# Kernel tuning notes

Hardware: AMD Instinct MI355X
Metric: run time of the kernel (lower is better)

The kernel has to match this reference:

```python
import jax, jax.numpy as jnp
import numpy as np

B, T, C = 16, 4096, 256


def setup_inputs() -> dict:
    key = jax.random.key(0)
    kx, kl = jax.random.split(key)
    x = jax.random.normal(kx, (B, T, C), dtype=jnp.float32)
    lengths = jax.random.randint(kl, (B,), T // 2, T + 1)  # valid lengths per sample
    pool_ranges = lengths  # region to pool over; k <= pool_range guaranteed by layer/total_layers choice
    return {
        "x": x,
        "lengths": lengths,
        "pool_ranges": pool_ranges,
        "top_k": 4,
        "layer": 1,
        "total_layers": 4,
    }


def _pool_one(xb, k, pool_range):
    # xb: [T, C]; keep, per column independently, the k largest values among the
    # first pool_range rows, preserving original row order (torch kmax_pooling).
    Trows, Ccols = xb.shape
    valid = jnp.arange(Trows) < pool_range            # [T]
    vals = jnp.where(valid[:, None], xb, -jnp.inf)    # mask invalid rows to rank last
    order = jnp.argsort(-vals, axis=0)                # descending order per column
    rank = jnp.argsort(order, axis=0)                 # inverse permutation = rank of each row
    keep = (rank < k) & valid[:, None]                # [T, C] which entries survive
    pos = jnp.cumsum(keep.astype(jnp.int32), axis=0) - 1  # compacted output row per column
    idx = jnp.where(keep, pos, Trows)                 # dropped entries -> dummy row Trows
    cols = jnp.arange(Ccols)[None, :]
    out = jnp.zeros((Trows + 1, Ccols), xb.dtype).at[idx, cols].set(
        jnp.where(keep, xb, jnp.zeros((), xb.dtype))
    )
    return out[:-1]                                   # [T, C]; rows >= k are zero padding


def reference(x, lengths, pool_ranges, top_k, layer, total_layers):
    # pool_target = max(top_k, ceil((total_layers - layer)/total_layers * length))
    num = total_layers - layer
    k = jnp.maximum(top_k, (num * lengths + total_layers - 1) // total_layers)
    k = jnp.minimum(k, pool_ranges)  # topk requires k <= available rows
    results = jax.vmap(_pool_one)(x, k, pool_ranges)  # [B, T, C], zero-padded past k_i
    pool_result_ranges = k
    return results, pool_result_ranges
```

## Files before the change

kernel.cpp:

```cpp
#include <hip/hip_runtime.h>
#include <stdint.h>


constexpr int T_ROWS = 4096;
constexpr int C_COLS = 256;
constexpr int NBATCH = 16;
constexpr int NSUB   = 8;
constexpr size_t NTOT = (size_t)NBATCH * T_ROWS * C_COLS;

__device__ __forceinline__ int compute_k(const int* lengths, const int* pool_ranges,
                                         const int* p_top_k, const int* p_layer,
                                         const int* p_total, int b, int* pr_out)
{
    int pr = pool_ranges[b];
    pr = pr < 0 ? 0 : (pr > T_ROWS ? T_ROWS : pr);
    const int len   = lengths[b];
    const int top_k = p_top_k[0];
    const int tot   = p_total[0];
    const int num   = tot - p_layer[0];
    int k = (num * len + tot - 1) / tot;
    if (k < top_k) k = top_k;
    if (k > pr)    k = pr;
    *pr_out = pr;
    return k;
}

__global__ __launch_bounds__(256)
void transpose_key_kernel(const float* __restrict__ x, uint32_t* __restrict__ xT)
{
    __shared__ uint32_t tile[64][65];
    const int bid = blockIdx.x;
    const int b   = bid >> 8;
    const int tt  = (bid >> 2) & 63;
    const int ct  = bid & 3;
    const int t0  = tt * 64, c0 = ct * 64;
    const int tid = threadIdx.x;
    const int qq  = tid & 15;
    const int rr  = tid >> 4;

    #pragma unroll
    for (int it = 0; it < 4; ++it) {
        const int r = it * 16 + rr;
        const float4 v = *reinterpret_cast<const float4*>(
            x + ((size_t)(b * T_ROWS + t0 + r) << 8) + c0 + qq * 4);
        const uint32_t w4[4] = {__float_as_uint(v.x), __float_as_uint(v.y),
                                __float_as_uint(v.z), __float_as_uint(v.w)};
        #pragma unroll
        for (int j = 0; j < 4; ++j)
            tile[qq * 4 + j][r] = w4[j] ^ ((w4[j] >> 31) ? 0xFFFFFFFFu : 0x80000000u);
    }
    __syncthreads();
    #pragma unroll
    for (int it = 0; it < 4; ++it) {
        const int cl = it * 16 + rr;
        uint4 o;
        o.x = tile[cl][qq * 4 + 0];
        o.y = tile[cl][qq * 4 + 1];
        o.z = tile[cl][qq * 4 + 2];
        o.w = tile[cl][qq * 4 + 3];
        *reinterpret_cast<uint4*>(
            xT + ((size_t)(b * C_COLS + c0 + cl) << 12) + t0 + qq * 4) = o;
    }
}

__global__ __launch_bounds__(256, 4)
void kmax_select_kernel(const uint32_t* __restrict__ xT,
                        const int* __restrict__ lengths,
                        const int* __restrict__ pool_ranges,
                        const int* __restrict__ p_top_k,
                        const int* __restrict__ p_layer,
                        const int* __restrict__ p_total,
                        float* __restrict__ out,
                        float* __restrict__ ws)
{
    __shared__ uint32_t hist[4][NSUB][256];

    const int t    = threadIdx.x;
    const int lane = t & 63;
    const int wid  = t >> 6;
    const int bid  = blockIdx.x;
    const int b    = bid >> 6;
    const int cg   = bid & 63;
    const int c    = cg * 4 + wid;

    int pr;
    const int k = compute_k(lengths, pool_ranges, p_top_k, p_layer, p_total, b, &pr);

    const uint4* cp = reinterpret_cast<const uint4*>(
                          xT + ((size_t)(b * C_COLS + c) << 12)) + lane;
    const int rb = lane * 4;
    uint32_t u[64];
    uint4 pf[4];
    #pragma unroll
    for (int i = 0; i < 4; ++i) pf[i] = cp[i * 64];
    #pragma unroll
    for (int i = 0; i < 16; ++i) {
        const uint4 v = pf[i & 3];
        if (i + 4 < 16) pf[i & 3] = cp[(i + 4) * 64];
        const int rowb = i * 256 + rb;
        u[i * 4 + 0] = (rowb + 0 < pr) ? v.x : 0u;
        u[i * 4 + 1] = (rowb + 1 < pr) ? v.y : 0u;
        u[i * 4 + 2] = (rowb + 2 < pr) ? v.z : 0u;
        u[i * 4 + 3] = (rowb + 3 < pr) ? v.w : 0u;
        asm("" : "+v"(u[i*4+0]), "+v"(u[i*4+1]), "+v"(u[i*4+2]), "+v"(u[i*4+3]));
    }

    if (k > 0) {
        uint32_t* hp = &hist[wid][0][0];
        uint32_t prefix = 0u, pmask = 0u, rem = (uint32_t)k;
        const uint32_t sub = lane & (NSUB - 1);

        #pragma unroll 1
        for (int pass = 0; pass < 4; ++pass) {
            const int shift = 24 - 8 * pass;
            uint4* hp4 = reinterpret_cast<uint4*>(hp);
            const uint4 z4 = make_uint4(0u, 0u, 0u, 0u);
            #pragma unroll
            for (int z = 0; z < 8; ++z) hp4[z * 64 + lane] = z4;
            #pragma unroll
            for (int m = 0; m < 64; ++m) {
                const uint32_t ui = u[m];
                if ((ui & pmask) == prefix)
                    atomicAdd(&hp[sub * 256 + (255u - ((ui >> shift) & 255u))], 1u);
            }
            uint32_t c4[4] = {0u, 0u, 0u, 0u};
            #pragma unroll
            for (int s = 0; s < NSUB; ++s) {
                const uint4 a = *reinterpret_cast<const uint4*>(&hp[s * 256 + 4 * lane]);
                c4[0] += a.x; c4[1] += a.y; c4[2] += a.z; c4[3] += a.w;
            }
            uint32_t loc[4], ssum = 0;
            #pragma unroll
            for (int q = 0; q < 4; ++q) { loc[q] = ssum; ssum += c4[q]; }
            uint32_t incl = ssum;
            #pragma unroll
            for (int off = 1; off < 64; off <<= 1) {
                const uint32_t nb = __shfl_up(incl, (unsigned)off, 64);
                if (lane >= off) incl += nb;
            }
            const uint32_t gexcl = incl - ssum;
            uint32_t sel = 0, nrem = 0;
            bool found = false;
            #pragma unroll
            for (int q = 0; q < 4; ++q) {
                const uint32_t sbb = gexcl + loc[q];
                if (sbb < rem && sbb + c4[q] >= rem) {
                    sel   = 255u - (uint32_t)(4 * lane + q);
                    nrem  = rem - sbb;
                    found = true;
                }
            }
            const unsigned long long fm = __ballot(found);
            const int src = __ffsll(fm) - 1;
            sel  = __shfl(sel,  src, 64);
            nrem = __shfl(nrem, src, 64);
            prefix |= sel << shift;
            pmask  |= 0xFFu << shift;
            rem = nrem;
        }

        const uint32_t th = prefix, tn = rem;
        uint32_t G = 0, E = 0;
        float* dst = ws + ((size_t)(b * C_COLS + c) << 12);
        #pragma unroll
        for (int i = 0; i < 16; ++i) {
            const int rowb = i * 256 + rb;
            uint32_t gt[4], eq[4], pk = 0;
            #pragma unroll
            for (int j = 0; j < 4; ++j) {
                const uint32_t ui = u[i * 4 + j];
                gt[j] = (ui > th) ? 1u : 0u;
                eq[j] = ((rowb + j < pr) && ui == th) ? 1u : 0u;
                pk += (gt[j] << 16) | eq[j];
            }
            uint32_t incl = pk;
            #pragma unroll
            for (int off = 1; off < 64; off <<= 1) {
                const uint32_t nb = __shfl_up(incl, (unsigned)off, 64);
                if (lane >= off) incl += nb;
            }
            const uint32_t tot  = __shfl(incl, 63, 64);
            const uint32_t base = incl - pk;
            uint32_t g = G + (base >> 16), e = E + (base & 0xFFFFu);
            #pragma unroll
            for (int j = 0; j < 4; ++j) {
                if (gt[j] || (eq[j] && e < tn)) {
                    const uint32_t pos  = g + (e < tn ? e : tn);
                    const uint32_t ui   = u[i * 4 + j];
                    const uint32_t bits = ui ^ ((ui >> 31) ? 0x80000000u : 0xFFFFFFFFu);
                    dst[pos] = __uint_as_float(bits);
                }
                g += gt[j];
                e += eq[j];
            }
            G += tot >> 16;
            E += tot & 0xFFFFu;
        }
    }

    if (cg == 0 && t == 0)
        out[NTOT + (size_t)b] = (float)k;
}

__global__ __launch_bounds__(256)
void finalize_kernel(const float* __restrict__ ws,
                     const int* __restrict__ lengths,
                     const int* __restrict__ pool_ranges,
                     const int* __restrict__ p_top_k,
                     const int* __restrict__ p_layer,
                     const int* __restrict__ p_total,
                     float* __restrict__ out)
{
    __shared__ float tile[64][65];
    const int bid  = blockIdx.x;
    const int b    = bid >> 8;
    const int pt   = (bid >> 2) & 63;
    const int ct   = bid & 3;
    const int pos0 = pt * 64, c0 = ct * 64;

    int pr;
    const int k = compute_k(lengths, pool_ranges, p_top_k, p_layer, p_total, b, &pr);

    const int tid = threadIdx.x;
    const int qq  = tid & 15;
    const int rr  = tid >> 4;
    float4* out4 = reinterpret_cast<float4*>(out);
    const float4 z4 = make_float4(0.f, 0.f, 0.f, 0.f);

    if (pos0 < k) {
        const float4* ws4 = reinterpret_cast<const float4*>(ws);
        #pragma unroll
        for (int it = 0; it < 4; ++it) {
            const int cl = it * 16 + rr;
            const float4 v = ws4[((size_t)(b * C_COLS + c0 + cl) << 10)
                                 + (pos0 >> 2) + qq];
            tile[cl][qq * 4 + 0] = v.x;
            tile[cl][qq * 4 + 1] = v.y;
            tile[cl][qq * 4 + 2] = v.z;
            tile[cl][qq * 4 + 3] = v.w;
        }
        __syncthreads();
        #pragma unroll
        for (int it = 0; it < 4; ++it) {
            const int r = it * 16 + rr;
            float4 v;
            v.x = tile[qq * 4 + 0][r];
            v.y = tile[qq * 4 + 1][r];
            v.z = tile[qq * 4 + 2][r];
            v.w = tile[qq * 4 + 3][r];
            if (pos0 + r >= k) v = z4;
            out4[((size_t)(b * T_ROWS + pos0 + r) << 6) + (c0 >> 2) + qq] = v;
        }
    } else {
        #pragma unroll
        for (int it = 0; it < 4; ++it) {
            const int r = it * 16 + rr;
            out4[((size_t)(b * T_ROWS + pos0 + r) << 6) + (c0 >> 2) + qq] = z4;
        }
    }
}

extern "C" void kernel_launch(void* const* d_in, const int* in_sizes, int n_in,
                              void* d_out, int out_size, void* d_ws, size_t ws_size,
                              hipStream_t stream)
{
    const float* x            = (const float*)d_in[0];
    const int*   lengths      = (const int*)d_in[1];
    const int*   pool_ranges  = (const int*)d_in[2];
    const int*   top_k        = (const int*)d_in[3];
    const int*   layer        = (const int*)d_in[4];
    const int*   total_layers = (const int*)d_in[5];
    float*       out          = (float*)d_out;
    float*       ws           = (float*)d_ws;

    hipLaunchKernelGGL(transpose_key_kernel, dim3(4096), dim3(256), 0, stream,
                       x, (uint32_t*)ws);
    hipLaunchKernelGGL(kmax_select_kernel, dim3(1024), dim3(256), 0, stream,
                       (const uint32_t*)ws, lengths, pool_ranges,
                       top_k, layer, total_layers, out, ws);
    hipLaunchKernelGGL(finalize_kernel, dim3(4096), dim3(256), 0, stream,
                       ws, lengths, pool_ranges, top_k, layer, total_layers, out);
}
```

Baseline: 90.70 us.

## Split each column's radix select across two wavefronts with shared histograms

Each column is now processed by two wavefronts (512-thread blocks), each holding half the rows in registers (32 values instead of 64). The two halves build a shared per-column histogram with block barriers. Sub-histogram selection now uses key bits rather than the lane id to spread atomics, and bins are rotated per column and sub-histogram to reduce LDS bank conflicts. The second half gets its compaction offset from a count reduced by the first half. This lowers register pressure and per-wave serial atomic work, and raises parallelism, at the cost of extra __syncthreads per pass.

```diff
diff --git a/kernel.cpp b/kernel.cpp
--- a/kernel.cpp
+++ b/kernel.cpp
@@ -6,6 +6,7 @@
 constexpr int C_COLS = 256;
 constexpr int NBATCH = 16;
 constexpr int NSUB   = 8;
+constexpr int SELBLK = 512;
 constexpr size_t NTOT = (size_t)NBATCH * T_ROWS * C_COLS;
 
 __device__ __forceinline__ int compute_k(const int* lengths, const int* pool_ranges,
@@ -63,7 +64,7 @@
     }
 }
 
-__global__ __launch_bounds__(256, 4)
+__global__ __launch_bounds__(SELBLK, 4)
 void kmax_select_kernel(const uint32_t* __restrict__ xT,
                         const int* __restrict__ lengths,
                         const int* __restrict__ pool_ranges,
@@ -74,30 +75,33 @@
                         float* __restrict__ ws)
 {
     __shared__ uint32_t hist[4][NSUB][256];
+    __shared__ uint32_t wtot[4];
 
     const int t    = threadIdx.x;
     const int lane = t & 63;
     const int wid  = t >> 6;
+    const int col  = wid >> 1;
+    const int half = wid & 1;
     const int bid  = blockIdx.x;
     const int b    = bid >> 6;
     const int cg   = bid & 63;
-    const int c    = cg * 4 + wid;
+    const int c    = cg * 4 + col;
 
     int pr;
     const int k = compute_k(lengths, pool_ranges, p_top_k, p_layer, p_total, b, &pr);
 
     const uint4* cp = reinterpret_cast<const uint4*>(
-                          xT + ((size_t)(b * C_COLS + c) << 12)) + lane;
-    const int rb = lane * 4;
-    uint32_t u[64];
+                          xT + ((size_t)(b * C_COLS + c) << 12)) + half * 512 + lane;
+    const int rb = half * 2048 + lane * 4;
+    uint32_t u[32];
     uint4 pf[4];
     #pragma unroll
     for (int i = 0; i < 4; ++i) pf[i] = cp[i * 64];
     #pragma unroll
-    for (int i = 0; i < 16; ++i) {
+    for (int i = 0; i < 8; ++i) {
         const uint4 v = pf[i & 3];
-        if (i + 4 < 16) pf[i & 3] = cp[(i + 4) * 64];
-        const int rowb = i * 256 + rb;
+        if (i + 4 < 8) pf[i & 3] = cp[(i + 4) * 64];
+        const int rowb = rb + i * 256;
         u[i * 4 + 0] = (rowb + 0 < pr) ? v.x : 0u;
         u[i * 4 + 1] = (rowb + 1 < pr) ? v.y : 0u;
         u[i * 4 + 2] = (rowb + 2 < pr) ? v.z : 0u;
@@ -105,28 +109,37 @@
         asm("" : "+v"(u[i*4+0]), "+v"(u[i*4+1]), "+v"(u[i*4+2]), "+v"(u[i*4+3]));
     }
 
+    uint32_t prefix = 0u, pmask = 0u, rem = (uint32_t)k;
     if (k > 0) {
-        uint32_t* hp = &hist[wid][0][0];
-        uint32_t prefix = 0u, pmask = 0u, rem = (uint32_t)k;
-        const uint32_t sub = lane & (NSUB - 1);
+        uint32_t* hp = &hist[col][0][0];
+        uint4*    hz = reinterpret_cast<uint4*>(hp) + half * 256;
+        const int colrot = 2 * col;
 
         #pragma unroll 1
         for (int pass = 0; pass < 4; ++pass) {
             const int shift = 24 - 8 * pass;
-            uint4* hp4 = reinterpret_cast<uint4*>(hp);
             const uint4 z4 = make_uint4(0u, 0u, 0u, 0u);
             #pragma unroll
-            for (int z = 0; z < 8; ++z) hp4[z * 64 + lane] = z4;
-            #pragma unroll
-            for (int m = 0; m < 64; ++m) {
+            for (int z = 0; z < 4; ++z) hz[z * 64 + lane] = z4;
+            __syncthreads();
+            #pragma unroll
+            for (int m = 0; m < 32; ++m) {
                 const uint32_t ui = u[m];
-                if ((ui & pmask) == prefix)
-                    atomicAdd(&hp[sub * 256 + (255u - ((ui >> shift) & 255u))], 1u);
-            }
+                if ((ui & pmask) == prefix) {
+                    const uint32_t bin = (ui >> shift) & 255u;
+                    const uint32_t sub = shift ? ((ui >> (shift - 3)) & 7u)
+                                               : ((uint32_t)lane & 7u);
+                    const uint32_t w = sub * 256u +
+                        (((255u - bin) + 4u * (sub + colrot)) & 255u);
+                    atomicAdd(&hp[w], 1u);
+                }
+            }
+            __syncthreads();
             uint32_t c4[4] = {0u, 0u, 0u, 0u};
             #pragma unroll
             for (int s = 0; s < NSUB; ++s) {
-                const uint4 a = *reinterpret_cast<const uint4*>(&hp[s * 256 + 4 * lane]);
+                const uint4 a = *reinterpret_cast<const uint4*>(
+                    &hp[s * 256 + 4 * ((lane + s + colrot) & 63)]);
                 c4[0] += a.x; c4[1] += a.y; c4[2] += a.z; c4[3] += a.w;
             }
             uint32_t loc[4], ssum = 0;
@@ -157,14 +170,31 @@
             prefix |= sel << shift;
             pmask  |= 0xFFu << shift;
             rem = nrem;
+            __syncthreads();
         }
 
         const uint32_t th = prefix, tn = rem;
-        uint32_t G = 0, E = 0;
+        if (half == 0) {
+            uint32_t pk = 0;
+            #pragma unroll
+            for (int m = 0; m < 32; ++m) {
+                const int rowb = rb + (m >> 2) * 256 + (m & 3);
+                const uint32_t ui = u[m];
+                pk += ((ui > th) ? 0x10000u : 0u)
+                    + (((rowb < pr) && ui == th) ? 1u : 0u);
+            }
+            #pragma unroll
+            for (int off = 32; off >= 1; off >>= 1) pk += __shfl_xor(pk, off, 64);
+            if (lane == 0) wtot[col] = pk;
+        }
+        __syncthreads();
+        const uint32_t base0 = half ? wtot[col] : 0u;
+
+        uint32_t G = base0 >> 16, E = base0 & 0xFFFFu;
         float* dst = ws + ((size_t)(b * C_COLS + c) << 12);
         #pragma unroll
-        for (int i = 0; i < 16; ++i) {
-            const int rowb = i * 256 + rb;
+        for (int i = 0; i < 8; ++i) {
+            const int rowb = rb + i * 256;
             uint32_t gt[4], eq[4], pk = 0;
             #pragma unroll
             for (int j = 0; j < 4; ++j) {
@@ -275,7 +305,7 @@
 
     hipLaunchKernelGGL(transpose_key_kernel, dim3(4096), dim3(256), 0, stream,
                        x, (uint32_t*)ws);
-    hipLaunchKernelGGL(kmax_select_kernel, dim3(1024), dim3(256), 0, stream,
+    hipLaunchKernelGGL(kmax_select_kernel, dim3(1024), dim3(SELBLK), 0, stream,
                        (const uint32_t*)ws, lengths, pool_ranges,
                        top_k, layer, total_layers, out, ws);
     hipLaunchKernelGGL(finalize_kernel, dim3(4096), dim3(256), 0, stream,
```

Measured after the change: 99.37 us. 1.1x slower.

## Re-stream column data from global each radix pass instead of holding it in registers

Applied to the files above, without the earlier changes.

Drops the 64-register per-thread cache of the column's values and reloads them from global memory (with prefetch) in each of the four radix-select passes and in the final compaction pass. Histogram sub-bins are now chosen from value bits, with a per-sub-bin rotated layout to spread LDS bank conflicts. Zeroing is folded into the histogram read-back. This frees registers for higher occupancy, in exchange for about five times the global or L2 read traffic per column.

```diff
diff --git a/kernel.cpp b/kernel.cpp
--- a/kernel.cpp
+++ b/kernel.cpp
@@ -86,48 +86,56 @@
     int pr;
     const int k = compute_k(lengths, pool_ranges, p_top_k, p_layer, p_total, b, &pr);
 
-    const uint4* cp = reinterpret_cast<const uint4*>(
-                          xT + ((size_t)(b * C_COLS + c) << 12)) + lane;
+    const size_t colbase = (size_t)(b * C_COLS + c) << 12;
+    const uint4* cp = reinterpret_cast<const uint4*>(xT + colbase) + lane;
     const int rb = lane * 4;
-    uint32_t u[64];
-    uint4 pf[4];
-    #pragma unroll
-    for (int i = 0; i < 4; ++i) pf[i] = cp[i * 64];
-    #pragma unroll
-    for (int i = 0; i < 16; ++i) {
-        const uint4 v = pf[i & 3];
-        if (i + 4 < 16) pf[i & 3] = cp[(i + 4) * 64];
-        const int rowb = i * 256 + rb;
-        u[i * 4 + 0] = (rowb + 0 < pr) ? v.x : 0u;
-        u[i * 4 + 1] = (rowb + 1 < pr) ? v.y : 0u;
-        u[i * 4 + 2] = (rowb + 2 < pr) ? v.z : 0u;
-        u[i * 4 + 3] = (rowb + 3 < pr) ? v.w : 0u;
-        asm("" : "+v"(u[i*4+0]), "+v"(u[i*4+1]), "+v"(u[i*4+2]), "+v"(u[i*4+3]));
-    }
 
     if (k > 0) {
         uint32_t* hp = &hist[wid][0][0];
+        {
+            uint4* hz = reinterpret_cast<uint4*>(hp);
+            const uint4 z4 = make_uint4(0u, 0u, 0u, 0u);
+            #pragma unroll
+            for (int z = 0; z < 8; ++z) hz[z * 64 + lane] = z4;
+        }
+
         uint32_t prefix = 0u, pmask = 0u, rem = (uint32_t)k;
-        const uint32_t sub = lane & (NSUB - 1);
 
         #pragma unroll 1
         for (int pass = 0; pass < 4; ++pass) {
-            const int shift = 24 - 8 * pass;
-            uint4* hp4 = reinterpret_cast<uint4*>(hp);
-            const uint4 z4 = make_uint4(0u, 0u, 0u, 0u);
-            #pragma unroll
-            for (int z = 0; z < 8; ++z) hp4[z * 64 + lane] = z4;
-            #pragma unroll
-            for (int m = 0; m < 64; ++m) {
-                const uint32_t ui = u[m];
-                if ((ui & pmask) == prefix)
-                    atomicAdd(&hp[sub * 256 + (255u - ((ui >> shift) & 255u))], 1u);
+            const int shift     = 24 - 8 * pass;
+            const int sub_shift = shift ? (shift - 3) : 0;
+            {
+                uint4 pf[4];
+                #pragma unroll
+                for (int i = 0; i < 4; ++i) pf[i] = cp[i * 64];
+                #pragma unroll
+                for (int i = 0; i < 16; ++i) {
+                    const uint4 v = pf[i & 3];
+                    if (i + 4 < 16) pf[i & 3] = cp[(i + 4) * 64];
+                    const int rowb = i * 256 + rb;
+                    const uint32_t raw[4] = {v.x, v.y, v.z, v.w};
+                    #pragma unroll
+                    for (int j = 0; j < 4; ++j) {
+                        const uint32_t ui = raw[j];
+                        if ((rowb + j < pr) && ((ui & pmask) == prefix)) {
+                            const uint32_t d   = 255u - ((ui >> shift) & 255u);
+                            const uint32_t sub = (ui >> sub_shift) & 7u;
+                            atomicAdd(&hp[sub * 256u + ((d + 4u * sub) & 255u)], 1u);
+                        }
+                    }
+                }
             }
             uint32_t c4[4] = {0u, 0u, 0u, 0u};
-            #pragma unroll
-            for (int s = 0; s < NSUB; ++s) {
-                const uint4 a = *reinterpret_cast<const uint4*>(&hp[s * 256 + 4 * lane]);
-                c4[0] += a.x; c4[1] += a.y; c4[2] += a.z; c4[3] += a.w;
+            {
+                const uint4 z4 = make_uint4(0u, 0u, 0u, 0u);
+                #pragma unroll
+                for (int s = 0; s < NSUB; ++s) {
+                    uint32_t* ap = &hp[s * 256u + ((4u * (uint32_t)lane + 4u * s) & 255u)];
+                    const uint4 a = *reinterpret_cast<const uint4*>(ap);
+                    *reinterpret_cast<uint4*>(ap) = z4;
+                    c4[0] += a.x; c4[1] += a.y; c4[2] += a.z; c4[3] += a.w;
+                }
             }
             uint32_t loc[4], ssum = 0;
             #pragma unroll
@@ -161,16 +169,22 @@
 
         const uint32_t th = prefix, tn = rem;
         uint32_t G = 0, E = 0;
-        float* dst = ws + ((size_t)(b * C_COLS + c) << 12);
+        float* dst = ws + colbase;
+        uint4 pf[4];
+        #pragma unroll
+        for (int i = 0; i < 4; ++i) pf[i] = cp[i * 64];
         #pragma unroll
         for (int i = 0; i < 16; ++i) {
+            const uint4 v = pf[i & 3];
+            if (i + 4 < 16) pf[i & 3] = cp[(i + 4) * 64];
             const int rowb = i * 256 + rb;
-            uint32_t gt[4], eq[4], pk = 0;
+            const uint32_t raw[4] = {v.x, v.y, v.z, v.w};
+            uint32_t gt[4], eq[4], pk = 0, uu[4];
             #pragma unroll
             for (int j = 0; j < 4; ++j) {
-                const uint32_t ui = u[i * 4 + j];
-                gt[j] = (ui > th) ? 1u : 0u;
-                eq[j] = ((rowb + j < pr) && ui == th) ? 1u : 0u;
+                uu[j] = (rowb + j < pr) ? raw[j] : 0u;
+                gt[j] = (uu[j] > th) ? 1u : 0u;
+                eq[j] = ((rowb + j < pr) && uu[j] == th) ? 1u : 0u;
                 pk += (gt[j] << 16) | eq[j];
             }
             uint32_t incl = pk;
@@ -186,8 +200,8 @@
             for (int j = 0; j < 4; ++j) {
                 if (gt[j] || (eq[j] && e < tn)) {
                     const uint32_t pos  = g + (e < tn ? e : tn);
-                    const uint32_t ui   = u[i * 4 + j];
-                    const uint32_t bits = ui ^ ((ui >> 31) ? 0x80000000u : 0xFFFFFFFFu);
+                    const uint32_t bits = uu[j] ^ ((uu[j] >> 31) ? 0x80000000u
+                                                                 : 0xFFFFFFFFu);
                     dst[pos] = __uint_as_float(bits);
                 }
                 g += gt[j];
```

New measurement: 95.18 us. 4.9% more time.
